# Performance work log

Hardware: AMD Instinct MI355X
Metric: run time of the kernel (lower is better)

The kernel has to match this reference:

```python
import jax, jax.numpy as jnp
import numpy as np

G = 4   # DCNv3 default groups
K = 3   # DCNv3 kernel size
P = K * K


def layernorm(x, g, b, eps=1e-5):
    m = jnp.mean(x, axis=-1, keepdims=True)
    v = jnp.var(x, axis=-1, keepdims=True)
    return (x - m) * jax.lax.rsqrt(v + eps) * g + b


def setup_inputs():
    key = jax.random.key(0)
    ks = jax.random.split(key, 12)
    B, Cin, C, H, W = 2, 64, 64, 512, 512
    s = lambda k, shape, sc=1.0: jax.random.normal(k, shape, jnp.float32) * sc
    return {
        "x": s(ks[0], (B, Cin, H, W)),
        "conv_w": s(ks[1], (C, Cin, 3, 3), 0.05),
        "w_in": s(ks[2], (C, C), 0.1), "b_in": s(ks[3], (C,), 0.1),
        "dw_w": s(ks[4], (3, 3, 1, C), 0.1), "dw_b": s(ks[5], (C,), 0.1),
        "ln_g": jnp.ones((C,), jnp.float32), "ln_b": jnp.zeros((C,), jnp.float32),
        "w_off": s(ks[6], (C, G * P * 2), 0.02), "b_off": s(ks[7], (G * P * 2,), 0.02),
        "w_mask": s(ks[8], (C, G * P), 0.1), "b_mask": s(ks[9], (G * P,), 0.1),
        "w_out": s(ks[10], (C, C), 0.1), "b_out": s(ks[11], (C,), 0.1),
    }


def dcnv3_core(x, offset, mask):
    # x: (N,H,W,C) projected input; offset: (N,H,W,G*P*2); mask: (N,H,W,G,P) softmaxed
    N, H, W, C = x.shape
    gc = C // G
    pad = 1
    xp = jnp.pad(x, ((0, 0), (pad, pad), (pad, pad), (0, 0)))
    Hin, Win = H + 2 * pad, W + 2 * pad
    dt = x.dtype
    # reference points: centers of each 3x3 window on the padded input, normalized
    ref_x = (jnp.arange(W, dtype=dt) + 1.5) / Win  # (dil*(k-1))//2 + 0.5 = 1.5
    ref_y = (jnp.arange(H, dtype=dt) + 1.5) / Hin
    # dilation grid: kx outer, ky inner (matches torch meshgrid 'ij' ordering)
    lin = jnp.arange(K, dtype=dt) - (K - 1) // 2
    gx, gy = jnp.meshgrid(lin, lin, indexing='ij')
    grid = jnp.stack([gx / Win, gy / Hin], -1).reshape(P, 2)  # identical for all groups
    off = offset.reshape(N, H, W, G, P, 2) / jnp.array([Win, Hin], dt)  # offset_scale=1
    loc_x = ref_x[None, None, :, None, None] + grid[:, 0] + off[..., 0]  # (N,H,W,G,P)
    loc_y = ref_y[None, :, None, None, None] + grid[:, 1] + off[..., 1]
    # grid_sample(align_corners=False): pixel = loc*size - 0.5, zero padding outside
    ix = loc_x * Win - 0.5
    iy = loc_y * Hin - 0.5
    x0f = jnp.floor(ix); y0f = jnp.floor(iy)
    fx = ix - x0f; fy = iy - y0f
    x0 = x0f.astype(jnp.int32); y0 = y0f.astype(jnp.int32)
    xg = xp.reshape(N, Hin * Win, G, gc)
    n_idx = jnp.arange(N)[:, None, None, None, None]
    g_idx = jnp.arange(G)[None, None, None, :, None]

    def corner(yc, xc, cw):
        valid = (yc >= 0) & (yc < Hin) & (xc >= 0) & (xc < Win)
        idx = jnp.clip(yc, 0, Hin - 1) * Win + jnp.clip(xc, 0, Win - 1)
        v = xg[n_idx, idx, g_idx]                     # (N,H,W,G,P,gc) irregular gather
        w = cw * valid.astype(dt) * mask              # fold mask into bilinear weight
        return jnp.einsum('nhwgpc,nhwgp->nhwgc', v, w)

    out = (corner(y0, x0, (1 - fy) * (1 - fx))
           + corner(y0, x0 + 1, (1 - fy) * fx)
           + corner(y0 + 1, x0, fy * (1 - fx))
           + corner(y0 + 1, x0 + 1, fy * fx))
    return out.reshape(N, H, W, C)


def reference(x, conv_w, w_in, b_in, dw_w, dw_b, ln_g, ln_b, w_off, b_off, w_mask, b_mask, w_out, b_out):
    # stride-2 'down' conv (no bias), then channels-last ReLU
    y = jax.lax.conv_general_dilated(x, conv_w, (2, 2), ((1, 1), (1, 1)),
                                     dimension_numbers=('NCHW', 'OIHW', 'NCHW'))
    y = jax.nn.relu(jnp.transpose(y, (0, 2, 3, 1)))  # (N,H,W,C)
    N, H, W, C = y.shape
    x_proj = y @ w_in + b_in                         # DCNv3 input_proj
    # depthwise 3x3 conv + LayerNorm + GELU for the offset/mask branch
    x1 = jax.lax.conv_general_dilated(y, dw_w, (1, 1), ((1, 1), (1, 1)),
                                      dimension_numbers=('NHWC', 'HWIO', 'NHWC'),
                                      feature_group_count=C) + dw_b
    x1 = jax.nn.gelu(layernorm(x1, ln_g, ln_b), approximate=False)
    offset = x1 @ w_off + b_off
    m = jax.nn.softmax((x1 @ w_mask + b_mask).reshape(N, H, W, G, P), axis=-1)
    out = dcnv3_core(x_proj, offset, m) @ w_out + b_out  # output_proj
    return jnp.transpose(out, (0, 3, 1, 2))  # back to NCHW
```

## Files before the change

### kernel.cpp

```cpp
#include <hip/hip_runtime.h>
#include <hip/hip_bf16.h>
#include <math.h>

#define NB 2
#define C 64
#define H 256
#define W 256
#define HIN 512
#define WIN 512
#define CIN 64
#define G 4
#define P 9
#define GC 16
#define NPIX (NB*H*W)

typedef __attribute__((ext_vector_type(8))) __bf16 bf16x8v;
typedef __attribute__((ext_vector_type(4))) float floatx4;

#define O_WOUT   47872
#define O_BIN    51968
#define O_DWW    52032
#define O_DWB    52608
#define O_LNG    52672
#define O_LNB    52736
#define O_BOFF   52800
#define O_BMASK  52872
#define O_BOUT   52908
#define O_WFRAG  53248
#define O_WINF   71680
#define O_WCOMB  73728
#define O_Y      77824
#define O_XP     (O_Y  + 8388608)
#define O_OFFS   (O_XP + 8388608)
#define O_MASK   (O_OFFS + 9437184)

static __device__ __forceinline__ unsigned pkbf(float a, float b) {
    unsigned lo = __bfloat16_as_ushort(__float2bfloat16(a));
    unsigned hi = __bfloat16_as_ushort(__float2bfloat16(b));
    return lo | (hi << 16);
}

__global__ void k_prep(const float* __restrict__ conv_w, const float* __restrict__ w_in,
                       const float* __restrict__ b_in,
                       const float* __restrict__ dw_w, const float* __restrict__ dw_b,
                       const float* __restrict__ ln_g, const float* __restrict__ ln_b,
                       const float* __restrict__ w_off, const float* __restrict__ b_off,
                       const float* __restrict__ w_mask, const float* __restrict__ b_mask,
                       const float* __restrict__ w_out, const float* __restrict__ b_out,
                       float* __restrict__ ws)
{
    int i = blockIdx.x*256 + threadIdx.x;
    if (i < 36864) {
        int j    = i & 7;
        int lane = (i >> 3) & 63;
        int nt   = (i >> 9) & 3;
        int ks   = (i >> 11) & 1;
        int tap  = i >> 12;
        int kh = tap / 3, kw = tap % 3;
        int ci = ks*32 + (lane >> 4)*8 + j;
        int co = nt*16 + (lane & 15);
        ((__hip_bfloat16*)(ws + O_WFRAG))[i] =
            __float2bfloat16(conv_w[co*576 + ci*9 + kh*3 + kw]);
    }
    if (i < 4096) {
        int j    = i & 7;
        int lane = (i >> 3) & 63;
        int s    = i >> 9;
        int nt   = s & 3, ks = s >> 2;
        int ci = ks*32 + (lane >> 4)*8 + j;
        int co = nt*16 + (lane & 15);
        ((__hip_bfloat16*)(ws + O_WINF))[i] = __float2bfloat16(w_in[ci*64 + co]);
    }
    if (i < 7168) {
        int j    = i & 7;
        int lane = (i >> 3) & 63;
        int s    = i >> 9;
        int nt   = s % 7, ks = s / 7;
        int ci = ks*32 + (lane >> 4)*8 + j;
        int jj = nt*16 + (lane & 15);
        float v = (jj < 72) ? w_off[ci*72 + jj] : (jj < 108 ? w_mask[ci*36 + (jj-72)] : 0.f);
        ((__hip_bfloat16*)(ws + O_WCOMB))[i] = __float2bfloat16(v);
    }
    if (i < 4096) ws[O_WOUT + i] = w_out[i];
    if (i < 64)   ws[O_BIN  + i] = b_in[i];
    if (i < 576)  ws[O_DWW  + i] = dw_w[i];
    if (i < 64)   ws[O_DWB  + i] = dw_b[i];
    if (i < 64)   ws[O_LNG  + i] = ln_g[i];
    if (i < 64)   ws[O_LNB  + i] = ln_b[i];
    if (i < 72)   ws[O_BOFF + i] = b_off[i];
    if (i < 36)   ws[O_BMASK+ i] = b_mask[i];
    if (i < 64)   ws[O_BOUT + i] = b_out[i];
}

__global__ __launch_bounds__(256) void k_xt(
    const float* __restrict__ x, __hip_bfloat16* __restrict__ xt)
{
    __shared__ float tile[64][65];
    int t = threadIdx.x;
    int b = blockIdx.x;
    int n  = b >> 12;
    int p0 = (b & 4095) * 64;
    const float* xb = x + (size_t)n*CIN*262144;
    #pragma unroll
    for (int k=0;k<16;k++) {
        int ch = k*4 + (t>>6);
        int px = t & 63;
        tile[px][ch] = xb[(size_t)ch*262144 + p0 + px];
    }
    __syncthreads();
    #pragma unroll
    for (int k=0;k<2;k++) {
        int e = k*256 + t;
        int px = e >> 3;
        int c8 = (e & 7)*8;
        __hip_bfloat16 v[8];
        #pragma unroll
        for (int j=0;j<8;j++) v[j] = __float2bfloat16(tile[px][c8+j]);
        *(uint4*)(xt + ((size_t)(n*262144 + p0 + px))*64 + c8) = *(uint4*)v;
    }
}

__global__ __launch_bounds__(256) void k_conv_mfma(
    const __hip_bfloat16* __restrict__ xt, const float* __restrict__ ws,
    float* __restrict__ y)
{
    const __hip_bfloat16* wf = (const __hip_bfloat16*)(ws + O_WFRAG);
    int t = threadIdx.x, lane = t & 63, wv = t >> 6;
    int pix0 = blockIdx.x*64 + wv*16;
    int n = pix0 >> 16;
    int hw = pix0 & 65535;
    int h = hw >> 8, wo0 = hw & 255;
    int m = lane & 15, q = lane >> 4;
    floatx4 acc[4] = {};
    #pragma unroll
    for (int kh=0; kh<3; kh++) {
        int ih = 2*h + kh - 1;
        if (ih < 0) continue;
        size_t rowbase = ((size_t)(n*512 + ih))*512;
        #pragma unroll
        for (int kw=0; kw<3; kw++) {
            int iw = 2*wo0 + kw - 1 + 2*m;
            bool inval = iw < 0;
            int iwc = inval ? 0 : iw;
            const __hip_bfloat16* ap = xt + (rowbase + iwc)*64 + q*8;
            const __hip_bfloat16* bp = wf + (kh*3 + kw)*4096 + lane*8;
            #pragma unroll
            for (int ks=0; ks<2; ks++) {
                uint4 au = *(const uint4*)(ap + ks*32);
                if (inval) au = make_uint4(0,0,0,0);
                bf16x8v av = __builtin_bit_cast(bf16x8v, au);
                #pragma unroll
                for (int nt=0; nt<4; nt++) {
                    uint4 bu = *(const uint4*)(bp + ks*2048 + nt*512);
                    bf16x8v bv = __builtin_bit_cast(bf16x8v, bu);
                    acc[nt] = __builtin_amdgcn_mfma_f32_16x16x32_bf16(av, bv, acc[nt], 0,0,0);
                }
            }
        }
    }
    int co0 = lane & 15;
    #pragma unroll
    for (int nt=0; nt<4; nt++)
        #pragma unroll
        for (int r=0; r<4; r++)
            y[((size_t)(pix0 + q*4 + r))*64 + nt*16 + co0] = fmaxf(acc[nt][r], 0.f);
}

__global__ __launch_bounds__(256) void k_branch(
    const float* __restrict__ y, const float* __restrict__ ws,
    float* __restrict__ offs, float* __restrict__ mask, float* __restrict__ xp)
{
    __shared__ float scr[64][68];
    __shared__ __align__(16) __hip_bfloat16 x1b[64][72];
    __shared__ __align__(16) __hip_bfloat16 ysb[64][72];
    int t = threadIdx.x;
    int lane = t & 63;
    int wv = t >> 6;
    int pix0 = blockIdx.x * 64;
    int n  = pix0 >> 16;
    int hw = pix0 & 65535;
    int hh = hw >> 8, ww0 = hw & 255;
    float dwv[9];
    #pragma unroll
    for (int k=0;k<9;k++) dwv[k] = ws[O_DWW + k*C + lane];
    float dbb = ws[O_DWB + lane];
    const float* ybase = y + (size_t)(n*H)*W*C + lane;
    #pragma unroll
    for (int rg=0; rg<4; rg++) {
        int i0 = wv*16 + rg*4;
        int cb = ww0 + i0 - 1;
        float cc[3][6];
        #pragma unroll
        for (int kh=0; kh<3; kh++) {
            int yh = hh + kh - 1;
            bool rv = (yh >= 0) && (yh < H);
            const float* yr = ybase + (size_t)(rv ? yh : 0)*W*C;
            #pragma unroll
            for (int c=0; c<6; c++) {
                int col = cb + c;
                bool ok = rv && (col >= 0) && (col < W);
                cc[kh][c] = ok ? yr[(ptrdiff_t)col*C] : 0.f;
            }
        }
        float a[4];
        #pragma unroll
        for (int u=0; u<4; u++) a[u] = dbb;
        #pragma unroll
        for (int kh=0; kh<3; kh++)
            #pragma unroll
            for (int kw=0; kw<3; kw++) {
                float wg = dwv[kh*3+kw];
                #pragma unroll
                for (int u=0; u<4; u++) a[u] = fmaf(cc[kh][u+kw], wg, a[u]);
            }
        #pragma unroll
        for (int u=0; u<4; u++) {
            scr[i0+u][lane] = a[u];
            ysb[i0+u][lane] = __float2bfloat16(cc[1][u+1]);
        }
    }
    asm volatile("" ::: "memory");
    {
        int pxl = lane >> 2;
        int cq  = lane & 3;
        int i   = wv*16 + pxl;
        const float* ar = &scr[i][cq*16];
        float4 V0 = *(const float4*)(ar);
        float4 V1 = *(const float4*)(ar + 4);
        float4 V2 = *(const float4*)(ar + 8);
        float4 V3 = *(const float4*)(ar + 12);
        float v[16] = {V0.x,V0.y,V0.z,V0.w, V1.x,V1.y,V1.z,V1.w,
                       V2.x,V2.y,V2.z,V2.w, V3.x,V3.y,V3.z,V3.w};
        float s = 0.f, s2 = 0.f;
        #pragma unroll
        for (int k=0;k<16;k++) { s += v[k]; s2 = fmaf(v[k], v[k], s2); }
        s  += __shfl_xor(s,  1, 64);  s  += __shfl_xor(s,  2, 64);
        s2 += __shfl_xor(s2, 1, 64);  s2 += __shfl_xor(s2, 2, 64);
        float mean = s * 0.015625f;
        float var  = fmaxf(fmaf(-mean, mean, s2 * 0.015625f), 0.f);
        float rsig = rsqrtf(var + 1e-5f);
        const float* gp = ws + O_LNG + cq*16;
        const float* bp = ws + O_LNB + cq*16;
        float4 Ga = *(const float4*)gp,      Gb = *(const float4*)(gp+4);
        float4 Gc = *(const float4*)(gp+8),  Gd = *(const float4*)(gp+12);
        float4 Ba = *(const float4*)bp,      Bb = *(const float4*)(bp+4);
        float4 Bc = *(const float4*)(bp+8),  Bd = *(const float4*)(bp+12);
        float gv[16] = {Ga.x,Ga.y,Ga.z,Ga.w, Gb.x,Gb.y,Gb.z,Gb.w,
                        Gc.x,Gc.y,Gc.z,Gc.w, Gd.x,Gd.y,Gd.z,Gd.w};
        float bv[16] = {Ba.x,Ba.y,Ba.z,Ba.w, Bb.x,Bb.y,Bb.z,Bb.w,
                        Bc.x,Bc.y,Bc.z,Bc.w, Bd.x,Bd.y,Bd.z,Bd.w};
        float gl[16];
        #pragma unroll
        for (int k=0;k<16;k++) {
            float xh = fmaf((v[k]-mean)*rsig, gv[k], bv[k]);
            gl[k] = 0.5f * xh * (1.f + erff(xh * 0.70710678118654752f));
        }
        uint4 w0, w1;
        w0.x = pkbf(gl[0],gl[1]);  w0.y = pkbf(gl[2],gl[3]);
        w0.z = pkbf(gl[4],gl[5]);  w0.w = pkbf(gl[6],gl[7]);
        w1.x = pkbf(gl[8],gl[9]);  w1.y = pkbf(gl[10],gl[11]);
        w1.z = pkbf(gl[12],gl[13]);w1.w = pkbf(gl[14],gl[15]);
        *(uint4*)&x1b[i][cq*16]     = w0;
        *(uint4*)&x1b[i][cq*16 + 8] = w1;
    }
    asm volatile("" ::: "memory");
    int m = lane & 15, q = lane >> 4;
    bf16x8v af[2];
    #pragma unroll
    for (int ks=0; ks<2; ks++)
        af[ks] = __builtin_bit_cast(bf16x8v, *(const uint4*)&x1b[wv*16 + m][ks*32 + q*8]);
    const __hip_bfloat16* wcomb = (const __hip_bfloat16*)(ws + O_WCOMB);
    #pragma unroll
    for (int nt=0; nt<7; nt++) {
        int j = nt*16 + m;
        float b = (j < 72) ? ws[O_BOFF + j] : (j < 108 ? ws[O_BMASK + j - 72] : 0.f);
        floatx4 acc = {b,b,b,b};
        #pragma unroll
        for (int ks=0; ks<2; ks++) {
            uint4 bu = *(const uint4*)(wcomb + (ks*7 + nt)*512 + lane*8);
            bf16x8v bvv = __builtin_bit_cast(bf16x8v, bu);
            acc = __builtin_amdgcn_mfma_f32_16x16x32_bf16(af[ks], bvv, acc, 0,0,0);
        }
        if (j < 72) {
            #pragma unroll
            for (int r=0;r<4;r++)
                offs[(size_t)(pix0 + wv*16 + q*4 + r)*72 + j] = acc[r];
        } else if (j < 108) {
            int jj = j - 72;
            int gg = jj / 9, qq = jj - gg*9;
            #pragma unroll
            for (int r=0;r<4;r++)
                scr[wv*16 + q*4 + r][gg*12 + qq] = acc[r];
        }
    }
    {
        const __hip_bfloat16* wfin = (const __hip_bfloat16*)(ws + O_WINF);
        bf16x8v af2[2];
        #pragma unroll
        for (int ks=0; ks<2; ks++) {
            uint4 u = *(const uint4*)&ysb[wv*16 + m][ks*32 + q*8];
            af2[ks] = __builtin_bit_cast(bf16x8v, u);
        }
        #pragma unroll
        for (int nt=0; nt<4; nt++) {
            float b = ws[O_BIN + nt*16 + m];
            floatx4 a2 = {b,b,b,b};
            #pragma unroll
            for (int ks=0; ks<2; ks++) {
                uint4 bu = *(const uint4*)(wfin + (ks*4 + nt)*512 + lane*8);
                bf16x8v bvv = __builtin_bit_cast(bf16x8v, bu);
                a2 = __builtin_amdgcn_mfma_f32_16x16x32_bf16(af2[ks], bvv, a2, 0,0,0);
            }
            #pragma unroll
            for (int r=0;r<4;r++)
                xp[((size_t)(pix0 + wv*16 + q*4 + r))*64 + nt*16 + m] = a2[r];
        }
    }
    asm volatile("" ::: "memory");
    {
        int pxl = lane >> 2;
        int i   = wv*16 + pxl;
        int g   = lane & 3;
        const float* lrow = &scr[i][g*12];
        float l[9];
        #pragma unroll
        for (int qq=0;qq<9;qq++) l[qq] = lrow[qq];
        float mx = l[0];
        #pragma unroll
        for (int qq=1;qq<9;qq++) mx = fmaxf(mx, l[qq]);
        float e[9]; float sum = 0.f;
        #pragma unroll
        for (int qq=0;qq<9;qq++) { e[qq] = expf(l[qq]-mx); sum += e[qq]; }
        float rs = 1.f / sum;
        float* mp = mask + (size_t)(pix0 + i)*36 + g*9;
        #pragma unroll
        for (int qq=0;qq<9;qq++) mp[qq] = e[qq] * rs;
    }
}

#define DPX 16
__global__ __launch_bounds__(256) void k_dcn(
    const float* __restrict__ xp, const float* __restrict__ offs,
    const float* __restrict__ mask, const float* __restrict__ ws,
    float* __restrict__ out)
{
    __shared__ float core[DPX][68];
    __shared__ float ot[64][17];
    __shared__ __align__(16) float offsl[DPX*72];
    __shared__ __align__(16) float maskl[DPX*36];
    const float* woutf = ws + O_WOUT;
    int t = threadIdx.x;
    int lane = t & 63;
    int wv = t >> 6;
    int bid = blockIdx.x;
    int nbk = (bid & 7) * (gridDim.x >> 3) + (bid >> 3);
    int pix0 = nbk * DPX;
    {
        const float4* osrc = (const float4*)(offs + (size_t)pix0*72);
        float4* odst = (float4*)offsl;
        odst[t] = osrc[t];
        if (t < 32) odst[256 + t] = osrc[256 + t];
        const float4* msrc = (const float4*)(mask + (size_t)pix0*36);
        float4* mdst = (float4*)maskl;
        if (t < 144) mdst[t] = msrc[t];
    }
    __syncthreads();
    int c4  = lane & 3;
    int g   = (lane >> 2) & 3;
    int sub = lane >> 4;
    int i   = wv*4 + sub;
    int pix = pix0 + i;
    int n  = pix >> 16;
    int hw = pix & 65535;
    int hh = hw >> 8, ww = hw & 255;
    const float* ob  = offsl + i*72 + g*18;
    const float* mb  = maskl + i*36 + g*9;
    const float* xpb = xp + (size_t)n*H*W*C + g*GC + c4*4;
    float4 acc = make_float4(0.f,0.f,0.f,0.f);
    #pragma unroll
    for (int p=0;p<P;p++) {
        int kx = p/3, ky = p%3;
        float2 o2 = *(const float2*)(ob + p*2);
        float offx = o2.x, offy = o2.y;
        float m = mb[p];
        float ix = (float)(ww + kx) + offx;
        float iy = (float)(hh + ky) + offy;
        float x0f = floorf(ix), y0f = floorf(iy);
        float fx = ix - x0f, fy = iy - y0f;
        int x0 = (int)x0f - 1, y0 = (int)y0f - 1;
        #pragma unroll
        for (int dy=0;dy<2;dy++) {
            int uy = y0 + dy;
            bool vy = (uy >= 0) & (uy < H);
            int uyc = min(max(uy,0), H-1);
            float wy = dy ? fy : (1.f - fy);
            #pragma unroll
            for (int dx=0;dx<2;dx++) {
                int ux = x0 + dx;
                bool vx = (ux >= 0) & (ux < W);
                int uxc = min(max(ux,0), W-1);
                float wx = dx ? fx : (1.f - fx);
                float wgt = (vy & vx) ? (wy*wx*m) : 0.f;
                const float4 v = *(const float4*)(xpb + ((size_t)uyc*W + uxc)*C);
                acc.x += v.x*wgt; acc.y += v.y*wgt;
                acc.z += v.z*wgt; acc.w += v.w*wgt;
            }
        }
    }
    *(float4*)&core[i][g*GC + c4*4] = acc;
    __syncthreads();
    {
        int cq = t & 15, px = t >> 4;
        float4 a = *(const float4*)(ws + O_BOUT + cq*4);
        #pragma unroll 4
        for (int c=0;c<64;c+=4) {
            float4 cv = *(const float4*)&core[px][c];
            const float* wp = woutf + c*64 + cq*4;
            float4 w0 = *(const float4*)(wp);
            float4 w1 = *(const float4*)(wp + 64);
            float4 w2 = *(const float4*)(wp + 128);
            float4 w3 = *(const float4*)(wp + 192);
            a.x += cv.x*w0.x + cv.y*w1.x + cv.z*w2.x + cv.w*w3.x;
            a.y += cv.x*w0.y + cv.y*w1.y + cv.z*w2.y + cv.w*w3.y;
            a.z += cv.x*w0.z + cv.y*w1.z + cv.z*w2.z + cv.w*w3.z;
            a.w += cv.x*w0.w + cv.y*w1.w + cv.z*w2.w + cv.w*w3.w;
        }
        ot[cq*4+0][px] = a.x;
        ot[cq*4+1][px] = a.y;
        ot[cq*4+2][px] = a.z;
        ot[cq*4+3][px] = a.w;
    }
    __syncthreads();
    {
        int n2 = pix0 >> 16, hw0 = pix0 & 65535;
        float* ob2 = out + (size_t)n2*C*65536 + hw0;
        #pragma unroll
        for (int k=0;k<4;k++) {
            int e = k*256 + t;
            int co = e >> 4, ppx = e & 15;
            ob2[(size_t)co*65536 + ppx] = ot[co][ppx];
        }
    }
}

extern "C" void kernel_launch(void* const* d_in, const int* in_sizes, int n_in,
                              void* d_out, int out_size, void* d_ws, size_t ws_size,
                              hipStream_t stream)
{
    const float* x     = (const float*)d_in[0];
    const float* convw = (const float*)d_in[1];
    const float* w_in  = (const float*)d_in[2];
    const float* b_in  = (const float*)d_in[3];
    const float* dw_w  = (const float*)d_in[4];
    const float* dw_b  = (const float*)d_in[5];
    const float* ln_g  = (const float*)d_in[6];
    const float* ln_b  = (const float*)d_in[7];
    const float* w_off = (const float*)d_in[8];
    const float* b_off = (const float*)d_in[9];
    const float* w_mask= (const float*)d_in[10];
    const float* b_mask= (const float*)d_in[11];
    const float* w_out = (const float*)d_in[12];
    const float* b_out = (const float*)d_in[13];

    float* ws   = (float*)d_ws;
    float* y    = ws + O_Y;
    float* xp   = ws + O_XP;
    float* offs = ws + O_OFFS;
    float* mask = ws + O_MASK;
    __hip_bfloat16* xt = (__hip_bfloat16*)(ws + O_XP);

    k_prep<<<144, 256, 0, stream>>>(convw, w_in, b_in, dw_w, dw_b, ln_g, ln_b,
                                    w_off, b_off, w_mask, b_mask, w_out, b_out, ws);
    k_xt<<<8192, 256, 0, stream>>>(x, xt);
    k_conv_mfma<<<2048, 256, 0, stream>>>(xt, ws, y);
    k_branch<<<NPIX/64, 256, 0, stream>>>(y, ws, offs, mask, xp);
    k_dcn<<<NPIX/DPX, 256, 0, stream>>>(xp, offs, mask, ws, (float*)d_out);
}
```

Before: 402.0 us.

## Stage output weights in LDS and batch DCN gather address/weight computation

The DCN kernel now copies the 64x64 output-projection weights into shared memory at block start instead of reading them from global memory in the projection loop. The bilinear sampling is split into two phases: first all 36 corner offsets and weights are computed, then all gathers are issued with two independent accumulator chains, exposing more memory-level parallelism. Launch bounds request 4 blocks per CU. The trade-offs are an extra 16KB of LDS and a 16KB weight load per 16-pixel block, plus higher register pressure from the precomputed arrays.

```diff
diff --git a/kernel.cpp b/kernel.cpp
--- a/kernel.cpp
+++ b/kernel.cpp
@@ -339,7 +339,7 @@
 }
 
 #define DPX 16
-__global__ __launch_bounds__(256) void k_dcn(
+__global__ __launch_bounds__(256, 4) void k_dcn(
     const float* __restrict__ xp, const float* __restrict__ offs,
     const float* __restrict__ mask, const float* __restrict__ ws,
     float* __restrict__ out)
@@ -348,7 +348,7 @@
     __shared__ float ot[64][17];
     __shared__ __align__(16) float offsl[DPX*72];
     __shared__ __align__(16) float maskl[DPX*36];
-    const float* woutf = ws + O_WOUT;
+    __shared__ __align__(16) float wsl[4096];
     int t = threadIdx.x;
     int lane = t & 63;
     int wv = t >> 6;
@@ -363,6 +363,10 @@
         const float4* msrc = (const float4*)(mask + (size_t)pix0*36);
         float4* mdst = (float4*)maskl;
         if (t < 144) mdst[t] = msrc[t];
+        const float4* wsrc = (const float4*)(ws + O_WOUT);
+        float4* wdst = (float4*)wsl;
+        #pragma unroll
+        for (int k=0;k<4;k++) wdst[k*256 + t] = wsrc[k*256 + t];
     }
     __syncthreads();
     int c4  = lane & 3;
@@ -376,37 +380,52 @@
     const float* ob  = offsl + i*72 + g*18;
     const float* mb  = maskl + i*36 + g*9;
     const float* xpb = xp + (size_t)n*H*W*C + g*GC + c4*4;
-    float4 acc = make_float4(0.f,0.f,0.f,0.f);
+    int   eo[P][4];
+    float wv4[P][4];
     #pragma unroll
     for (int p=0;p<P;p++) {
-        int kx = p/3, ky = p%3;
-        float2 o2 = *(const float2*)(ob + p*2);
-        float offx = o2.x, offy = o2.y;
-        float m = mb[p];
+        const int kx = p/3, ky = p%3;
+        float offx = ob[p*2], offy = ob[p*2+1];
+        float mm = mb[p];
         float ix = (float)(ww + kx) + offx;
         float iy = (float)(hh + ky) + offy;
         float x0f = floorf(ix), y0f = floorf(iy);
         float fx = ix - x0f, fy = iy - y0f;
         int x0 = (int)x0f - 1, y0 = (int)y0f - 1;
-        #pragma unroll
-        for (int dy=0;dy<2;dy++) {
-            int uy = y0 + dy;
-            bool vy = (uy >= 0) & (uy < H);
-            int uyc = min(max(uy,0), H-1);
-            float wy = dy ? fy : (1.f - fy);
-            #pragma unroll
-            for (int dx=0;dx<2;dx++) {
-                int ux = x0 + dx;
-                bool vx = (ux >= 0) & (ux < W);
-                int uxc = min(max(ux,0), W-1);
-                float wx = dx ? fx : (1.f - fx);
-                float wgt = (vy & vx) ? (wy*wx*m) : 0.f;
-                const float4 v = *(const float4*)(xpb + ((size_t)uyc*W + uxc)*C);
-                acc.x += v.x*wgt; acc.y += v.y*wgt;
-                acc.z += v.z*wgt; acc.w += v.w*wgt;
-            }
-        }
-    }
+        int x1 = x0 + 1,       y1 = y0 + 1;
+        bool vx0 = (x0 >= 0) & (x0 < W), vx1 = (x1 >= 0) & (x1 < W);
+        bool vy0 = (y0 >= 0) & (y0 < H), vy1 = (y1 >= 0) & (y1 < H);
+        int cx0 = min(max(x0,0), W-1), cx1 = min(max(x1,0), W-1);
+        int ry0 = min(max(y0,0), H-1) * W, ry1 = min(max(y1,0), H-1) * W;
+        float am = (1.f - fy) * mm, bm = fy * mm;
+        float fxc = 1.f - fx;
+        eo[p][0] = (ry0 + cx0) * C;  wv4[p][0] = (vy0 & vx0) ? am * fxc : 0.f;
+        eo[p][1] = (ry0 + cx1) * C;  wv4[p][1] = (vy0 & vx1) ? am * fx  : 0.f;
+        eo[p][2] = (ry1 + cx0) * C;  wv4[p][2] = (vy1 & vx0) ? bm * fxc : 0.f;
+        eo[p][3] = (ry1 + cx1) * C;  wv4[p][3] = (vy1 & vx1) ? bm * fx  : 0.f;
+    }
+    floatx4 ac0 = {0.f,0.f,0.f,0.f}, ac1 = {0.f,0.f,0.f,0.f};
+    #pragma unroll
+    for (int p=0;p<P;p++) {
+        float4 v0 = *(const float4*)(xpb + eo[p][0]);
+        float4 v1 = *(const float4*)(xpb + eo[p][1]);
+        float4 v2 = *(const float4*)(xpb + eo[p][2]);
+        float4 v3 = *(const float4*)(xpb + eo[p][3]);
+        float w0 = wv4[p][0], w1 = wv4[p][1], w2 = wv4[p][2], w3 = wv4[p][3];
+        ac0[0] = fmaf(v0.x, w0, fmaf(v1.x, w1, ac0[0]));
+        ac0[1] = fmaf(v0.y, w0, fmaf(v1.y, w1, ac0[1]));
+        ac0[2] = fmaf(v0.z, w0, fmaf(v1.z, w1, ac0[2]));
+        ac0[3] = fmaf(v0.w, w0, fmaf(v1.w, w1, ac0[3]));
+        ac1[0] = fmaf(v2.x, w2, fmaf(v3.x, w3, ac1[0]));
+        ac1[1] = fmaf(v2.y, w2, fmaf(v3.y, w3, ac1[1]));
+        ac1[2] = fmaf(v2.z, w2, fmaf(v3.z, w3, ac1[2]));
+        ac1[3] = fmaf(v2.w, w2, fmaf(v3.w, w3, ac1[3]));
+    }
+    float4 acc;
+    acc.x = ac0[0] + ac1[0];
+    acc.y = ac0[1] + ac1[1];
+    acc.z = ac0[2] + ac1[2];
+    acc.w = ac0[3] + ac1[3];
     *(float4*)&core[i][g*GC + c4*4] = acc;
     __syncthreads();
     {
@@ -415,7 +434,7 @@
         #pragma unroll 4
         for (int c=0;c<64;c+=4) {
             float4 cv = *(const float4*)&core[px][c];
-            const float* wp = woutf + c*64 + cq*4;
+            const float* wp = wsl + c*64 + cq*4;
             float4 w0 = *(const float4*)(wp);
             float4 w1 = *(const float4*)(wp + 64);
             float4 w2 = *(const float4*)(wp + 128);
```

Result: faster. 362.5 us (-9.8%).
